# Kernel optimization log

Measured on AMD Instinct MI355X. Metric: run time of the kernel, lower is better.

The kernel has to match this reference:

```python
import jax, jax.numpy as jnp
import numpy as np

N = 100_000      # nodes
E = 1_600_000    # directed edges
G = 512          # graphs in batch
IN, H, C = 26, 64, 2
EPS = 1e-5       # BatchNorm eps (torch default)


def setup_inputs() -> dict:
    key = jax.random.key(0)
    ks = jax.random.split(key, 12)
    s = 0.1
    return {
        "x": jax.random.normal(ks[0], (N, IN), jnp.float32),
        "edge_row": jax.random.randint(ks[1], (E,), 0, N, jnp.int32),
        "edge_col": jax.random.randint(ks[2], (E,), 0, N, jnp.int32),
        "batch": jnp.sort(jax.random.randint(ks[3], (N,), 0, G, jnp.int32)),
        "W0": jax.random.normal(ks[4], (IN, H), jnp.float32) * s,
        "b0": jnp.zeros((H,), jnp.float32),
        "W1": jax.random.normal(ks[5], (H, H), jnp.float32) * s,
        "b1": jnp.zeros((H,), jnp.float32),
        "W2": jax.random.normal(ks[6], (H, H), jnp.float32) * s,
        "b2": jnp.zeros((H,), jnp.float32),
        "bn_g": jnp.ones((3, H), jnp.float32),
        "bn_b": jnp.zeros((3, H), jnp.float32),
        "bn_m": jnp.zeros((3, H), jnp.float32),
        "bn_v": jnp.ones((3, H), jnp.float32),
        "Wc1": jax.random.normal(ks[7], (2 * H, H), jnp.float32) * s,
        "bc1": jnp.zeros((H,), jnp.float32),
        "Wc2": jax.random.normal(ks[8], (H, C), jnp.float32) * s,
        "bc2": jnp.zeros((C,), jnp.float32),
    }


def reference(x, edge_row, edge_col, batch, W0, b0, W1, b1, W2, b2,
              bn_g, bn_b, bn_m, bn_v, Wc1, bc1, Wc2, bc2):
    n = x.shape[0]
    # GCN normalization with self-loops (PyG gcn_norm)
    sl = jnp.arange(n, dtype=edge_row.dtype)
    row = jnp.concatenate([edge_row, sl])  # sources j
    col = jnp.concatenate([edge_col, sl])  # targets i
    deg = jax.ops.segment_sum(jnp.ones_like(row, jnp.float32), col, num_segments=n)
    dinv = jnp.where(deg > 0, jax.lax.rsqrt(deg), 0.0)
    norm = dinv[row] * dinv[col]  # [E+N]

    def conv(h, W, b):
        h = h @ W                                   # transform first (PyG)
        msg = h[row] * norm[:, None]                # gather + scale
        return jax.ops.segment_sum(msg, col, num_segments=n) + b  # scatter-add

    h = x
    for i, (W, b) in enumerate([(W0, b0), (W1, b1), (W2, b2)]):
        h = conv(h, W, b)
        # BatchNorm (eval: running stats) + ReLU; dropout off at inference
        h = (h - bn_m[i]) * jax.lax.rsqrt(bn_v[i] + EPS) * bn_g[i] + bn_b[i]
        h = jax.nn.relu(h)

    # global mean + max pool over batch vector
    cnt = jax.ops.segment_sum(jnp.ones((n, 1), h.dtype), batch, num_segments=G)
    mean = jax.ops.segment_sum(h, batch, num_segments=G) / jnp.maximum(cnt, 1.0)
    mx = jax.ops.segment_max(h, batch, num_segments=G)
    pooled = jnp.concatenate([mean, mx], axis=1)    # [G, 2H]

    hid = jax.nn.relu(pooled @ Wc1 + bc1)
    return hid @ Wc2 + bc2                          # [G, C]
```

## Files before the change

### kernel.cpp

```cpp
#include <hip/hip_runtime.h>

#define HDIM 64
#define EPSBN 1e-5f
#define MNODES 8
#define CAP 48
#define NB 64
#define BCAP 26624
#define EPB 4096
#define PBB 32

typedef unsigned short u16;

__device__ __forceinline__ float bf2f(u16 b) {
    return __uint_as_float(((unsigned)b) << 16);
}
__device__ __forceinline__ u16 f2bf_rne(float f) {
    unsigned u = __float_as_uint(f);
    u += 0x7FFFu + ((u >> 16) & 1u);
    return (u16)(u >> 16);
}

__global__ __launch_bounds__(256) void bucket_k(
    const int* __restrict__ row, const int* __restrict__ col,
    int* __restrict__ gcnt, int2* __restrict__ bstore, int E, int N) {
    __shared__ int hist[NB];
    __shared__ int cur[NB];
    int tid = threadIdx.x;
    if (tid < NB) hist[tid] = 0;
    __syncthreads();
    int e0 = blockIdx.x * EPB;
    for (int u = 0; u < EPB / 256; u++) {
        int e = e0 + u * 256 + tid;
        if (e < E) {
            int c = __builtin_nontemporal_load(&col[e]);
            int b = (int)(((unsigned long long)c * NB) / (unsigned)N);
            atomicAdd(&hist[b], 1);
        }
    }
    __syncthreads();
    if (tid < NB) cur[tid] = atomicAdd(&gcnt[tid], hist[tid]);
    __syncthreads();
    for (int u = 0; u < EPB / 256; u++) {
        int e = e0 + u * 256 + tid;
        if (e < E) {
            int c = __builtin_nontemporal_load(&col[e]);
            int r = __builtin_nontemporal_load(&row[e]);
            int b = (int)(((unsigned long long)c * NB) / (unsigned)N);
            int slot = atomicAdd(&cur[b], 1);
            if (slot < BCAP) bstore[(size_t)b * BCAP + slot] = make_int2(r, c);
        }
    }
}

__global__ __launch_bounds__(256) void csrfill_k(
    const int* __restrict__ gcnt, const int2* __restrict__ bstore,
    int* __restrict__ cnt, int* __restrict__ esrcP) {
    int b = blockIdx.x / PBB;
    int sub = blockIdx.x % PBB;
    int M = min(gcnt[b], BCAP);
    const int2* bs = bstore + (size_t)b * BCAP;
    for (int k = sub * 256 + threadIdx.x; k < M; k += PBB * 256) {
        int2 rc = bs[k];
        int rank = atomicAdd(&cnt[rc.y], 1);
        if (rank < CAP) esrcP[rc.y * CAP + rank] = rc.x;
    }
}

__global__ void prep_k(const int* __restrict__ cnt, float* __restrict__ dinv,
                       const float* __restrict__ x, u16* __restrict__ xp,
                       const int* __restrict__ batch, int* __restrict__ bounds,
                       int INR, int N, int G) {
    int idx = blockIdx.x * blockDim.x + threadIdx.x;
    if (idx >= N * 32) return;
    int i = idx >> 5, k = idx & 31;
    float di = rsqrtf((float)cnt[i] + 1.0f);
    if (k == 0) {
        dinv[i] = di;
        int b = batch[i];
        int bp = (i == 0) ? -1 : batch[i - 1];
        for (int g = bp + 1; g <= b; g++) bounds[g] = i;
        if (i == N - 1) { for (int g = b + 1; g <= G; g++) bounds[g] = N; }
    }
    float xv = (k < INR) ? __builtin_nontemporal_load(&x[i * INR + k]) : 0.f;
    xp[idx] = f2bf_rne(di * xv);
}

template <int KIN, bool SCALEOUT>
__global__ __launch_bounds__(64) void conv_k(
    const u16* __restrict__ hb, const int* __restrict__ cnt,
    const int* __restrict__ esrcP, const float* __restrict__ dinv,
    const float* __restrict__ W, int KINR,
    const float* __restrict__ bias, const float* __restrict__ g,
    const float* __restrict__ bb, const float* __restrict__ m,
    const float* __restrict__ v, void* __restrict__ hout_, int n) {
    int lane = threadIdx.x;
    float wreg[KIN];
#pragma unroll
    for (int k = 0; k < KIN; k++) wreg[k] = (k < KINR) ? W[k * HDIM + lane] : 0.f;
    const float sc = g[lane] * rsqrtf(v[lane] + EPSBN);
    const float sh = (bias[lane] - m[lane]) * sc + bb[lane];

    __shared__ float agg4[4][KIN];

    const int feat = lane & (KIN - 1);
    auto ldh = [&](int node) -> float {
        return bf2f(hb[(size_t)node * KIN + feat]);
    };

    for (int grp = 0; grp < 2; grp++) {
        int ibase = blockIdx.x * MNODES + grp * 4;
        if (ibase >= n) break;
        float acc0 = 0.f, acc1 = 0.f, acc2 = 0.f, acc3 = 0.f;
        int e0 = 0, n0 = 0, e1 = 0, n1 = 0, e2 = 0, n2 = 0, e3 = 0, n3 = 0;
        {
            acc0 = ldh(ibase); e0 = ibase * CAP; n0 = e0 + min(cnt[ibase], CAP);
            if (ibase + 1 < n) { acc1 = ldh(ibase + 1); e1 = (ibase + 1) * CAP; n1 = e1 + min(cnt[ibase + 1], CAP); }
            if (ibase + 2 < n) { acc2 = ldh(ibase + 2); e2 = (ibase + 2) * CAP; n2 = e2 + min(cnt[ibase + 2], CAP); }
            if (ibase + 3 < n) { acc3 = ldh(ibase + 3); e3 = (ibase + 3) * CAP; n3 = e3 + min(cnt[ibase + 3], CAP); }
        }
        while (e0 + 2 <= n0 && e1 + 2 <= n1 && e2 + 2 <= n2 && e3 + 2 <= n3) {
            int s00 = esrcP[e0], s01 = esrcP[e0 + 1];
            int s10 = esrcP[e1], s11 = esrcP[e1 + 1];
            int s20 = esrcP[e2], s21 = esrcP[e2 + 1];
            int s30 = esrcP[e3], s31 = esrcP[e3 + 1];
            float h00 = ldh(s00), h01 = ldh(s01);
            float h10 = ldh(s10), h11 = ldh(s11);
            float h20 = ldh(s20), h21 = ldh(s21);
            float h30 = ldh(s30), h31 = ldh(s31);
            acc0 += h00 + h01;
            acc1 += h10 + h11;
            acc2 += h20 + h21;
            acc3 += h30 + h31;
            e0 += 2; e1 += 2; e2 += 2; e3 += 2;
        }
#define DRAIN(ek, nk, ak)                                                     \
        for (; ek + 4 <= nk; ek += 4) {                                       \
            int a = esrcP[ek], b = esrcP[ek + 1], c = esrcP[ek + 2], d = esrcP[ek + 3]; \
            float ha = ldh(a), hb2 = ldh(b), hc = ldh(c), hd = ldh(d);        \
            ak += (ha + hb2) + (hc + hd);                                     \
        }                                                                     \
        for (; ek < nk; ek++) ak += ldh(esrcP[ek]);
        DRAIN(e0, n0, acc0)
        DRAIN(e1, n1, acc1)
        DRAIN(e2, n2, acc2)
        DRAIN(e3, n3, acc3)
#undef DRAIN

        __syncthreads();
        if (lane < KIN) {
            agg4[0][lane] = acc0; agg4[1][lane] = acc1;
            agg4[2][lane] = acc2; agg4[3][lane] = acc3;
        }
        __syncthreads();
        for (int q = 0; q < 4; q++) {
            int i = ibase + q;
            if (i >= n) break;
            float di = dinv[i];
            float dot = 0.f;
            const float4* aggv = (const float4*)agg4[q];
#pragma unroll
            for (int k4 = 0; k4 < KIN / 4; k4++) {
                float4 a = aggv[k4];
                dot = fmaf(a.x, wreg[4 * k4 + 0], dot);
                dot = fmaf(a.y, wreg[4 * k4 + 1], dot);
                dot = fmaf(a.z, wreg[4 * k4 + 2], dot);
                dot = fmaf(a.w, wreg[4 * k4 + 3], dot);
            }
            float y = fmaxf(fmaf(dot * di, sc, sh), 0.f);
            if (SCALEOUT) ((u16*)hout_)[(size_t)i * HDIM + lane] = f2bf_rne(di * y);
            else          ((float*)hout_)[(size_t)i * HDIM + lane] = y;
        }
    }
}

__global__ __launch_bounds__(256) void pool_mlp_k(
    const float* __restrict__ h, const int* __restrict__ bounds,
    const float* __restrict__ Wc1, const float* __restrict__ bc1,
    const float* __restrict__ Wc2, const float* __restrict__ bc2,
    float* __restrict__ out, int n) {
    int gidx = blockIdx.x;
    int tid = threadIdx.x;
    int lane = tid & 63;
    int wv = tid >> 6;

    int start = bounds[gidx], end = bounds[gidx + 1];

    float sum = 0.f, mx = 0.f;
    for (int i = start + wv; i < end; i += 4) {
        float val = h[(size_t)i * HDIM + lane];
        sum += val;
        mx = fmaxf(mx, val);
    }
    __shared__ float ssum[4 * HDIM];
    __shared__ float smax[4 * HDIM];
    __shared__ float pooled[2 * HDIM];
    ssum[wv * HDIM + lane] = sum;
    smax[wv * HDIM + lane] = mx;
    __syncthreads();
    if (wv == 0) {
        float sv = ssum[lane] + ssum[64 + lane] + ssum[128 + lane] + ssum[192 + lane];
        float mm = fmaxf(fmaxf(smax[lane], smax[64 + lane]),
                         fmaxf(smax[128 + lane], smax[192 + lane]));
        int cntg = end - start;
        pooled[lane] = sv / fmaxf((float)cntg, 1.f);
        pooled[HDIM + lane] = mm;
    }
    __syncthreads();
    if (wv == 0) {
        float a = bc1[lane];
#pragma unroll
        for (int k = 0; k < 2 * HDIM; k++) a = fmaf(pooled[k], Wc1[k * HDIM + lane], a);
        a = fmaxf(a, 0.f);
#pragma unroll
        for (int c = 0; c < 2; c++) {
            float vv = a * Wc2[lane * 2 + c];
            for (int off = 32; off; off >>= 1) vv += __shfl_down(vv, off);
            if (lane == 0) out[gidx * 2 + c] = vv + bc2[c];
        }
    }
}

extern "C" void kernel_launch(void* const* d_in, const int* in_sizes, int n_in,
                              void* d_out, int out_size, void* d_ws, size_t ws_size,
                              hipStream_t stream) {
    const float* x    = (const float*)d_in[0];
    const int*   erow = (const int*)d_in[1];
    const int*   ecol = (const int*)d_in[2];
    const int*   batch= (const int*)d_in[3];
    const float* W0   = (const float*)d_in[4];
    const float* b0   = (const float*)d_in[5];
    const float* W1   = (const float*)d_in[6];
    const float* b1   = (const float*)d_in[7];
    const float* W2   = (const float*)d_in[8];
    const float* b2   = (const float*)d_in[9];
    const float* bn_g = (const float*)d_in[10];
    const float* bn_b = (const float*)d_in[11];
    const float* bn_m = (const float*)d_in[12];
    const float* bn_v = (const float*)d_in[13];
    const float* Wc1  = (const float*)d_in[14];
    const float* bc1  = (const float*)d_in[15];
    const float* Wc2  = (const float*)d_in[16];
    const float* bc2  = (const float*)d_in[17];
    float* out = (float*)d_out;

    const int N = in_sizes[3];
    const int E = in_sizes[1];
    const int G = out_size / 2;
    const int INR = in_sizes[0] / N;

    char* ws = (char*)d_ws;
    size_t off = 0;
    auto alloc = [&](size_t bytes) -> void* {
        void* p = ws + off;
        off += (bytes + 255) & ~(size_t)255;
        return p;
    };
    int*   cntAll = (int*)alloc((size_t)(N + NB) * 4);
    int*   cnt    = cntAll;
    int*   gcnt   = cntAll + N;
    float* dinv   = (float*)alloc((size_t)N * 4);
    int*   bounds = (int*)alloc((size_t)(512 + 1) * 4);
    int2*  bstore = (int2*)alloc((size_t)NB * BCAP * 8);
    int*   esrcP  = (int*)alloc((size_t)N * CAP * 4);
    void*  bufA   = alloc((size_t)N * HDIM * 4);
    void*  bufB   = alloc((size_t)N * HDIM * 4);
    (void)ws_size;

    hipMemsetAsync(cntAll, 0, (size_t)(N + NB) * 4, stream);
    bucket_k<<<(E + EPB - 1) / EPB, 256, 0, stream>>>(erow, ecol, gcnt, bstore, E, N);
    csrfill_k<<<NB * PBB, 256, 0, stream>>>(gcnt, bstore, cnt, esrcP);
    prep_k<<<(N * 32 + 255) / 256, 256, 0, stream>>>(cnt, dinv, x, (u16*)bufB,
                                                     batch, bounds, INR, N, G);

    int cgrid = (N + MNODES - 1) / MNODES;
    conv_k<32, true><<<cgrid, 64, 0, stream>>>((const u16*)bufB, cnt, esrcP, dinv, W0, INR, b0,
        bn_g + 0, bn_b + 0, bn_m + 0, bn_v + 0, bufA, N);
    conv_k<64, true><<<cgrid, 64, 0, stream>>>((const u16*)bufA, cnt, esrcP, dinv, W1, 64, b1,
        bn_g + 64, bn_b + 64, bn_m + 64, bn_v + 64, bufB, N);
    conv_k<64, false><<<cgrid, 64, 0, stream>>>((const u16*)bufB, cnt, esrcP, dinv, W2, 64, b2,
        bn_g + 128, bn_b + 128, bn_m + 128, bn_v + 128, bufA, N);

    pool_mlp_k<<<G, 256, 0, stream>>>((const float*)bufA, bounds, Wc1, bc1, Wc2, bc2, out, N);
}
```

Baseline: 470.5 us.

## Count CSR degrees in shared memory per bucket and fuse prep into bucketing

Edges are now split into 256 destination-range buckets instead of 64, each sized to a contiguous node range. One block per bucket builds its slot lists with shared-memory atomics instead of global atomics on the per-node count array. The degree normalisation and bf16 input scaling move into that same kernel, and the graph-bounds computation moves into the bucketing kernel. This drops one kernel launch and most of the count-array memset, but the fill phase now runs with only 256 blocks, so each block carries more serial work.

After: 423.9 us. 9.9% less time.

```diff
diff --git a/kernel.cpp b/kernel.cpp
--- a/kernel.cpp
+++ b/kernel.cpp
@@ -4,10 +4,10 @@
 #define EPSBN 1e-5f
 #define MNODES 8
 #define CAP 48
-#define NB 64
-#define BCAP 26624
-#define EPB 4096
-#define PBB 32
+#define NB 256
+#define BCAP 8192
+#define EPB 2048
+#define MAXW 400
 
 typedef unsigned short u16;
 
@@ -20,13 +20,24 @@
     return (u16)(u >> 16);
 }
 
+__device__ __forceinline__ int bstart_of(int b, int N) {
+    return (int)(((long long)b * N + NB - 1) / NB);
+}
+
 __global__ __launch_bounds__(256) void bucket_k(
     const int* __restrict__ row, const int* __restrict__ col,
-    int* __restrict__ gcnt, int2* __restrict__ bstore, int E, int N) {
+    int* __restrict__ gcnt, int2* __restrict__ bstore, int E, int N,
+    const int* __restrict__ batch, int* __restrict__ bounds, int G) {
     __shared__ int hist[NB];
     __shared__ int cur[NB];
     int tid = threadIdx.x;
-    if (tid < NB) hist[tid] = 0;
+    hist[tid] = 0;
+    for (int i = blockIdx.x * 256 + tid; i < N; i += gridDim.x * 256) {
+        int b = batch[i];
+        int bp = (i == 0) ? -1 : batch[i - 1];
+        for (int g = bp + 1; g <= b; g++) bounds[g] = i;
+        if (i == N - 1) { for (int g = b + 1; g <= G; g++) bounds[g] = N; }
+    }
     __syncthreads();
     int e0 = blockIdx.x * EPB;
     for (int u = 0; u < EPB / 256; u++) {
@@ -38,7 +49,7 @@
         }
     }
     __syncthreads();
-    if (tid < NB) cur[tid] = atomicAdd(&gcnt[tid], hist[tid]);
+    cur[tid] = atomicAdd(&gcnt[tid], hist[tid]);
     __syncthreads();
     for (int u = 0; u < EPB / 256; u++) {
         int e = e0 + u * 256 + tid;
@@ -54,35 +65,33 @@
 
 __global__ __launch_bounds__(256) void csrfill_k(
     const int* __restrict__ gcnt, const int2* __restrict__ bstore,
-    int* __restrict__ cnt, int* __restrict__ esrcP) {
-    int b = blockIdx.x / PBB;
-    int sub = blockIdx.x % PBB;
+    int* __restrict__ cnt, int* __restrict__ esrcP,
+    float* __restrict__ dinv, const float* __restrict__ x,
+    u16* __restrict__ xp, int INR, int N) {
+    __shared__ int lcnt[MAXW];
+    int b = blockIdx.x, tid = threadIdx.x;
+    int bs = bstart_of(b, N);
+    int be = bstart_of(b + 1, N);
+    int width = be - bs;
+    for (int t = tid; t < width; t += 256) lcnt[t] = 0;
+    __syncthreads();
     int M = min(gcnt[b], BCAP);
-    const int2* bs = bstore + (size_t)b * BCAP;
-    for (int k = sub * 256 + threadIdx.x; k < M; k += PBB * 256) {
-        int2 rc = bs[k];
-        int rank = atomicAdd(&cnt[rc.y], 1);
+    const int2* bsp = bstore + (size_t)b * BCAP;
+    for (int k = tid; k < M; k += 256) {
+        int2 rc = bsp[k];
+        int rank = atomicAdd(&lcnt[rc.y - bs], 1);
         if (rank < CAP) esrcP[rc.y * CAP + rank] = rc.x;
     }
-}
-
-__global__ void prep_k(const int* __restrict__ cnt, float* __restrict__ dinv,
-                       const float* __restrict__ x, u16* __restrict__ xp,
-                       const int* __restrict__ batch, int* __restrict__ bounds,
-                       int INR, int N, int G) {
-    int idx = blockIdx.x * blockDim.x + threadIdx.x;
-    if (idx >= N * 32) return;
-    int i = idx >> 5, k = idx & 31;
-    float di = rsqrtf((float)cnt[i] + 1.0f);
-    if (k == 0) {
-        dinv[i] = di;
-        int b = batch[i];
-        int bp = (i == 0) ? -1 : batch[i - 1];
-        for (int g = bp + 1; g <= b; g++) bounds[g] = i;
-        if (i == N - 1) { for (int g = b + 1; g <= G; g++) bounds[g] = N; }
-    }
-    float xv = (k < INR) ? __builtin_nontemporal_load(&x[i * INR + k]) : 0.f;
-    xp[idx] = f2bf_rne(di * xv);
+    __syncthreads();
+    for (int t = tid; t < width; t += 256) cnt[bs + t] = lcnt[t];
+    for (int idx = tid; idx < width * 32; idx += 256) {
+        int tl = idx >> 5, k = idx & 31;
+        int i = bs + tl;
+        float di = rsqrtf((float)min(lcnt[tl], CAP) + 1.0f);
+        if (k == 0) dinv[i] = di;
+        float xv = (k < INR) ? __builtin_nontemporal_load(&x[i * INR + k]) : 0.f;
+        xp[i * 32 + k] = f2bf_rne(di * xv);
+    }
 }
 
 template <int KIN, bool SCALEOUT>
@@ -255,9 +264,8 @@
         off += (bytes + 255) & ~(size_t)255;
         return p;
     };
-    int*   cntAll = (int*)alloc((size_t)(N + NB) * 4);
-    int*   cnt    = cntAll;
-    int*   gcnt   = cntAll + N;
+    int*   gcnt   = (int*)alloc(NB * 4);
+    int*   cnt    = (int*)alloc((size_t)N * 4);
     float* dinv   = (float*)alloc((size_t)N * 4);
     int*   bounds = (int*)alloc((size_t)(512 + 1) * 4);
     int2*  bstore = (int2*)alloc((size_t)NB * BCAP * 8);
@@ -266,11 +274,10 @@
     void*  bufB   = alloc((size_t)N * HDIM * 4);
     (void)ws_size;
 
-    hipMemsetAsync(cntAll, 0, (size_t)(N + NB) * 4, stream);
-    bucket_k<<<(E + EPB - 1) / EPB, 256, 0, stream>>>(erow, ecol, gcnt, bstore, E, N);
-    csrfill_k<<<NB * PBB, 256, 0, stream>>>(gcnt, bstore, cnt, esrcP);
-    prep_k<<<(N * 32 + 255) / 256, 256, 0, stream>>>(cnt, dinv, x, (u16*)bufB,
-                                                     batch, bounds, INR, N, G);
+    hipMemsetAsync(gcnt, 0, NB * 4, stream);
+    int nbk = (E + EPB - 1) / EPB;
+    bucket_k<<<nbk, 256, 0, stream>>>(erow, ecol, gcnt, bstore, E, N, batch, bounds, G);
+    csrfill_k<<<NB, 256, 0, stream>>>(gcnt, bstore, cnt, esrcP, dinv, x, (u16*)bufB, INR, N);
 
     int cgrid = (N + MNODES - 1) / MNODES;
     conv_k<32, true><<<cgrid, 64, 0, stream>>>((const u16*)bufB, cnt, esrcP, dinv, W0, INR, b0,
```
